# Performance work log

Hardware: AMD Instinct MI355X
Metric: run time of the kernel (lower is better)

## Reference

```python
import jax, jax.numpy as jnp
import numpy as np

NUM_HEADS = 16


def setup_inputs() -> dict:
    key = jax.random.key(0)
    ks = jax.random.split(key, 9)
    B, N, E = 2, 2048, 1024
    s = 1.0 / np.sqrt(E).astype(np.float32)
    inp = {"x": jax.random.normal(ks[0], (B, N, E), jnp.float32)}
    names = ["q", "k", "v", "o"]
    for i, n in enumerate(names):
        inp[f"W{n}"] = jax.random.normal(ks[1 + 2 * i], (E, E), jnp.float32) * s
        inp[f"b{n}"] = jax.random.normal(ks[2 + 2 * i], (E,), jnp.float32) * 0.01
    return inp


def _feature(x):
    # act_fun = '1+elu'
    return jax.nn.elu(x) + 1.0


def reference(x, Wq, bq, Wk, bk, Wv, bv, Wo, bo):
    B, N, E = x.shape
    H = NUM_HEADS
    d = E // H

    def proj(t, W, b):  # torch nn.Linear: t @ W^T + b
        return t @ W.T + b

    def split_heads(t):  # (B,N,E) -> (B,H,N,d)
        return t.reshape(B, N, H, d).transpose(0, 2, 1, 3)

    q = _feature(split_heads(proj(x, Wq, bq)))
    k = _feature(split_heads(proj(x, Wk, bk)))
    v = split_heads(proj(x, Wv, bv))

    # causal linear attention: o_t = q_t @ cumsum_{s<=t} (k_s v_s^T)
    kv = jnp.cumsum(k[..., :, None] * v[..., None, :], axis=2)  # (B,H,N,d,d)
    o = jnp.einsum('bhnd,bhnde->bhne', q, kv)                   # (B,H,N,d)

    o = o.transpose(0, 2, 1, 3).reshape(B, N, E)
    return o @ Wo.T + bo
```

## Files before the change

kernel.cpp:

```cpp
#include <hip/hip_runtime.h>
#include <hip/hip_bf16.h>
#include <cmath>

typedef unsigned short u16;
typedef __bf16 bf16x8 __attribute__((ext_vector_type(8)));
typedef float  f32x4  __attribute__((ext_vector_type(4)));
typedef float  f4     __attribute__((ext_vector_type(4)));
typedef u16    us4    __attribute__((ext_vector_type(4)));

#define DEVFN __device__ __forceinline__

static constexpr int Bq = 2, Nq = 2048, Eq = 1024;
static constexpr int Mq = Bq * Nq;
static constexpr int CHK = 64;
static constexpr int NC  = Nq / CHK;
static constexpr int BH  = Bq * 16;

DEVFN u16 f2b(float f) {
    union { float f; unsigned int u; } x; x.f = f;
    unsigned int r = x.u + 0x7fffu + ((x.u >> 16) & 1u);
    return (u16)(r >> 16);
}

DEVFN void gl_lds16(const u16* g, u16* l) {
    __builtin_amdgcn_global_load_lds(
        (const __attribute__((address_space(1))) unsigned int*)(g),
        (__attribute__((address_space(3))) unsigned int*)(l),
        16, 0, 0);
}

DEVFN const bf16x8* frag(const u16* S, int R, int G) {
    return reinterpret_cast<const bf16x8*>(&S[R * 64 + ((G ^ (R & 7)) << 3)]);
}

__global__ __launch_bounds__(256) void cvt_kernel(const float* __restrict__ src,
                                                  u16* __restrict__ dst, int n4) {
    int i = blockIdx.x * 256 + threadIdx.x;
    if (i < n4) {
        f4 v = *reinterpret_cast<const f4*>(&src[(size_t)i * 4]);
        us4 p; p[0] = f2b(v[0]); p[1] = f2b(v[1]); p[2] = f2b(v[2]); p[3] = f2b(v[3]);
        *reinterpret_cast<us4*>(&dst[(size_t)i * 4]) = p;
    }
}

__global__ __launch_bounds__(256) void cvt4_kernel(const float* __restrict__ s0,
                                                   const float* __restrict__ s1,
                                                   const float* __restrict__ s2,
                                                   const float* __restrict__ s3,
                                                   u16* __restrict__ dst, int n4each) {
    const int which = blockIdx.y;
    const float* s = (which == 0) ? s0 : (which == 1) ? s1 : (which == 2) ? s2 : s3;
    int i = blockIdx.x * 256 + threadIdx.x;
    if (i < n4each) {
        f4 v = *reinterpret_cast<const f4*>(&s[(size_t)i * 4]);
        us4 p; p[0] = f2b(v[0]); p[1] = f2b(v[1]); p[2] = f2b(v[2]); p[3] = f2b(v[3]);
        *reinterpret_cast<us4*>(&dst[((size_t)which * n4each + i) * 4]) = p;
    }
}

template<int MODE>
__global__ __launch_bounds__(256)
void gemm_kernel(const u16* __restrict__ X, const u16* __restrict__ W,
                 const float* __restrict__ b0, const float* __restrict__ b1,
                 const float* __restrict__ b2,
                 u16* __restrict__ Qb, u16* __restrict__ Kb, u16* __restrict__ KbT,
                 u16* __restrict__ VbT, float* __restrict__ outF)
{
    constexpr int BM = (MODE == 0) ? 128 : 64;
    constexpr int MI = BM / 32;
    __shared__ u16 As[BM * 64];
    __shared__ u16 Bs[128 * 64];
    const int tid  = threadIdx.x;
    const int m0   = blockIdx.y * BM, n0 = blockIdx.x * 128;
    const int wid  = tid >> 6, lane = tid & 63;
    const int wr   = (wid >> 1) * (BM / 2), wc = (wid & 1) * 64;
    const int fr   = lane & 15, fq = lane >> 4;

    const int srow = tid >> 3;
    const int sw   = (tid & 7) ^ (srow & 7);
    const u16* gA = X + (size_t)(m0 + srow) * 1024 + sw * 8;
    const u16* gB = W + (size_t)(n0 + srow) * 1024 + sw * 8;
    u16* lA = As + wid * 512;
    u16* lB = Bs + wid * 512;

    f32x4 acc[MI][4] = {};

    for (int k0 = 0; k0 < 1024; k0 += 64) {
        __syncthreads();
#pragma unroll
        for (int i = 0; i < BM / 32; ++i)
            gl_lds16(gA + k0 + i * 32 * 1024, lA + i * 2048);
#pragma unroll
        for (int i = 0; i < 4; ++i)
            gl_lds16(gB + k0 + i * 32 * 1024, lB + i * 2048);
        __syncthreads();

#pragma unroll
        for (int kk = 0; kk < 2; ++kk) {
            bf16x8 af[MI], bfv[4];
#pragma unroll
            for (int mi = 0; mi < MI; ++mi)
                af[mi] = *frag(As, wr + mi * 16 + fr, kk * 4 + fq);
#pragma unroll
            for (int ni = 0; ni < 4; ++ni)
                bfv[ni] = *frag(Bs, wc + ni * 16 + fr, kk * 4 + fq);
#pragma unroll
            for (int mi = 0; mi < MI; ++mi)
#pragma unroll
                for (int ni = 0; ni < 4; ++ni)
                    acc[mi][ni] = __builtin_amdgcn_mfma_f32_16x16x32_bf16(
                        af[mi], bfv[ni], acc[mi][ni], 0, 0, 0);
        }
    }

    if (MODE == 0) {
        const int seg = n0 >> 10;
        const float* bp = (seg == 0) ? b0 : (seg == 1) ? b1 : b2;
#pragma unroll
        for (int mi = 0; mi < MI; ++mi)
#pragma unroll
            for (int ni = 0; ni < 4; ++ni) {
                const int nl    = (n0 & 1023) + wc + ni * 16 + fr;
                const int mbase = m0 + wr + mi * 16 + fq * 4;
                const float bn  = bp[nl];
                float vr[4];
#pragma unroll
                for (int r = 0; r < 4; ++r) {
                    float v = acc[mi][ni][r] + bn;
                    if (seg < 2) v = (v > 0.f) ? (v + 1.f) : __expf(v);
                    vr[r] = v;
                }
                if (seg == 0) {
#pragma unroll
                    for (int r = 0; r < 4; ++r)
                        Qb[(size_t)(mbase + r) * 1024 + nl] = f2b(vr[r]);
                } else {
                    us4 pk;
#pragma unroll
                    for (int r = 0; r < 4; ++r) pk[r] = f2b(vr[r]);
                    const int bb = mbase >> 11, nt = mbase & 2047;
                    const int hh = nl >> 6,     dd = nl & 63;
                    u16* T = (seg == 1) ? KbT : VbT;
                    *reinterpret_cast<us4*>(
                        &T[((size_t)(bb * 16 + hh) * 64 + dd) * 2048 + nt]) = pk;
                    if (seg == 1) {
#pragma unroll
                        for (int r = 0; r < 4; ++r)
                            Kb[(size_t)(mbase + r) * 1024 + nl] = f2b(vr[r]);
                    }
                }
            }
    } else {
#pragma unroll
        for (int mi = 0; mi < MI; ++mi)
#pragma unroll
            for (int ni = 0; ni < 4; ++ni) {
                const int n     = n0 + wc + ni * 16 + fr;
                const int mbase = m0 + wr + mi * 16 + fq * 4;
                const float bn  = b0[n];
#pragma unroll
                for (int r = 0; r < 4; ++r)
                    outF[(size_t)(mbase + r) * 1024 + n] = acc[mi][ni][r] + bn;
            }
    }
}

__global__ __launch_bounds__(64)
void chunk_kv_kernel(const u16* __restrict__ KbT, const u16* __restrict__ VbT,
                     float* __restrict__ KVT)
{
    const int blk = blockIdx.x;
    const int bh = blk >> 5, c = blk & 31;
    const int lane = threadIdx.x;
    const int fr = lane & 15, fq = lane >> 4, fk = fq * 8;
    const u16* kt = KbT + (size_t)bh * 64 * 2048;
    const u16* vt = VbT + (size_t)bh * 64 * 2048;

    bf16x8 a[4][2], b[4][2];
#pragma unroll
    for (int mi = 0; mi < 4; ++mi)
#pragma unroll
        for (int kh = 0; kh < 2; ++kh)
            a[mi][kh] = *reinterpret_cast<const bf16x8*>(
                &vt[(size_t)(mi * 16 + fr) * 2048 + c * 64 + kh * 32 + fk]);
#pragma unroll
    for (int ni = 0; ni < 4; ++ni)
#pragma unroll
        for (int kh = 0; kh < 2; ++kh)
            b[ni][kh] = *reinterpret_cast<const bf16x8*>(
                &kt[(size_t)(ni * 16 + fr) * 2048 + c * 64 + kh * 32 + fk]);

    f32x4 acc[4][4] = {};
#pragma unroll
    for (int mi = 0; mi < 4; ++mi)
#pragma unroll
        for (int ni = 0; ni < 4; ++ni)
#pragma unroll
            for (int kh = 0; kh < 2; ++kh)
                acc[mi][ni] = __builtin_amdgcn_mfma_f32_16x16x32_bf16(
                    a[mi][kh], b[ni][kh], acc[mi][ni], 0, 0, 0);

    float* out = KVT + (size_t)blk * 4096;
#pragma unroll
    for (int mi = 0; mi < 4; ++mi)
#pragma unroll
        for (int ni = 0; ni < 4; ++ni)
#pragma unroll
            for (int r = 0; r < 4; ++r)
                out[(mi * 16 + fq * 4 + r) * 64 + ni * 16 + fr] = acc[mi][ni][r];
}

__global__ __launch_bounds__(256)
void scan_kernel(const float* __restrict__ KVT, u16* __restrict__ STb)
{
    const int bh = blockIdx.x >> 4, sl = blockIdx.x & 15;
    const int el = sl * 256 + threadIdx.x;
    const float* src = KVT + (size_t)bh * NC * 4096 + el;
    u16*         dst = STb + (size_t)bh * NC * 4096 + el;
    float run = 0.f;
#pragma unroll 4
    for (int c = 0; c < NC; ++c) {
        dst[(size_t)c * 4096] = f2b(run);
        run += src[(size_t)c * 4096];
    }
}

__global__ __launch_bounds__(64)
void attn_kernel(const u16* __restrict__ Qb, const u16* __restrict__ Kb,
                 const u16* __restrict__ VbT, const u16* __restrict__ STb,
                 u16* __restrict__ Ob)
{
    __shared__ u16 P[64 * 72];
    const int blk = blockIdx.x;
    const int bh = blk >> 5, c = blk & 31;
    const int b = bh >> 4, h = bh & 15;
    const int lane = threadIdx.x;
    const int fr = lane & 15, fq = lane >> 4, fk = fq * 8;
    const int tok0 = b * 2048 + c * 64;

    bf16x8 qa[4][2];
#pragma unroll
    for (int mi = 0; mi < 4; ++mi)
#pragma unroll
        for (int kh = 0; kh < 2; ++kh)
            qa[mi][kh] = *reinterpret_cast<const bf16x8*>(
                &Qb[(size_t)(tok0 + mi * 16 + fr) * 1024 + h * 64 + kh * 32 + fk]);

    {
        bf16x8 kb[4][2];
#pragma unroll
        for (int si = 0; si < 4; ++si)
#pragma unroll
            for (int kh = 0; kh < 2; ++kh)
                kb[si][kh] = *reinterpret_cast<const bf16x8*>(
                    &Kb[(size_t)(tok0 + si * 16 + fr) * 1024 + h * 64 + kh * 32 + fk]);
        f32x4 p[4][4] = {};
#pragma unroll
        for (int mi = 0; mi < 4; ++mi)
#pragma unroll
            for (int si = 0; si < 4; ++si)
#pragma unroll
                for (int kh = 0; kh < 2; ++kh)
                    p[mi][si] = __builtin_amdgcn_mfma_f32_16x16x32_bf16(
                        qa[mi][kh], kb[si][kh], p[mi][si], 0, 0, 0);
#pragma unroll
        for (int mi = 0; mi < 4; ++mi)
#pragma unroll
            for (int si = 0; si < 4; ++si)
#pragma unroll
                for (int r = 0; r < 4; ++r) {
                    int t = mi * 16 + fq * 4 + r;
                    int s = si * 16 + fr;
                    float v = (s <= t) ? p[mi][si][r] : 0.0f;
                    P[t * 72 + s] = f2b(v);
                }
    }
    __syncthreads();

    f32x4 acc[4][4] = {};
    {
        const u16* st = STb + (size_t)blk * 4096;
        bf16x8 sb[4][2];
#pragma unroll
        for (int ni = 0; ni < 4; ++ni)
#pragma unroll
            for (int kh = 0; kh < 2; ++kh)
                sb[ni][kh] = *reinterpret_cast<const bf16x8*>(
                    &st[(ni * 16 + fr) * 64 + kh * 32 + fk]);
#pragma unroll
        for (int mi = 0; mi < 4; ++mi)
#pragma unroll
            for (int ni = 0; ni < 4; ++ni)
#pragma unroll
                for (int kh = 0; kh < 2; ++kh)
                    acc[mi][ni] = __builtin_amdgcn_mfma_f32_16x16x32_bf16(
                        qa[mi][kh], sb[ni][kh], acc[mi][ni], 0, 0, 0);
    }
    {
        const u16* vt = VbT + (size_t)bh * 64 * 2048;
#pragma unroll
        for (int sh = 0; sh < 2; ++sh) {
            bf16x8 pa[4], vb[4];
#pragma unroll
            for (int mi = 0; mi < 4; ++mi)
                pa[mi] = *reinterpret_cast<const bf16x8*>(
                    &P[(mi * 16 + fr) * 72 + sh * 32 + fk]);
#pragma unroll
            for (int ni = 0; ni < 4; ++ni)
                vb[ni] = *reinterpret_cast<const bf16x8*>(
                    &vt[(size_t)(ni * 16 + fr) * 2048 + c * 64 + sh * 32 + fk]);
#pragma unroll
            for (int mi = 0; mi < 4; ++mi)
#pragma unroll
                for (int ni = 0; ni < 4; ++ni)
                    acc[mi][ni] = __builtin_amdgcn_mfma_f32_16x16x32_bf16(
                        pa[mi], vb[ni], acc[mi][ni], 0, 0, 0);
        }
    }
#pragma unroll
    for (int mi = 0; mi < 4; ++mi)
#pragma unroll
        for (int ni = 0; ni < 4; ++ni)
#pragma unroll
            for (int r = 0; r < 4; ++r) {
                int t = tok0 + mi * 16 + fq * 4 + r;
                int n = h * 64 + ni * 16 + fr;
                Ob[(size_t)t * 1024 + n] = f2b(acc[mi][ni][r]);
            }
}

extern "C" void kernel_launch(void* const* d_in, const int* in_sizes, int n_in,
                              void* d_out, int out_size, void* d_ws, size_t ws_size,
                              hipStream_t stream)
{
    (void)in_sizes; (void)n_in; (void)out_size; (void)ws_size;
    const float* x  = (const float*)d_in[0];
    const float* Wq = (const float*)d_in[1];
    const float* bq = (const float*)d_in[2];
    const float* Wk = (const float*)d_in[3];
    const float* bk = (const float*)d_in[4];
    const float* Wv = (const float*)d_in[5];
    const float* bv = (const float*)d_in[6];
    const float* Wo = (const float*)d_in[7];
    const float* bo = (const float*)d_in[8];
    float* out = (float*)d_out;

    char* ws = (char*)d_ws;
    constexpr size_t SZ_ME = (size_t)Mq * Eq * 2;
    u16*   Qb  = (u16*)  (ws + 0 * SZ_ME);
    u16*   Kb  = (u16*)  (ws + 1 * SZ_ME);
    u16*   KbT = (u16*)  (ws + 2 * SZ_ME);
    u16*   VbT = (u16*)  (ws + 3 * SZ_ME);
    u16*   Ob  = (u16*)  (ws + 4 * SZ_ME);
    float* KVT = (float*)(ws + 5 * SZ_ME);
    u16*   STb = (u16*)  (ws + 5 * SZ_ME + (size_t)BH * NC * 4096 * 4);
    u16*   Xb  = (u16*)  (ws + 6 * SZ_ME + (size_t)BH * NC * 4096 * 4);
    u16*   Wb0 = (u16*)  (ws + 7 * SZ_ME + (size_t)BH * NC * 4096 * 4);
    u16* Wqkvb = Wb0;
    u16* Wob   = Wb0 + (size_t)3 * Eq * Eq;

    {
        int n4x = Mq * Eq / 4;
        cvt_kernel<<<dim3((n4x + 255) / 256), dim3(256), 0, stream>>>(x, Xb, n4x);
        int n4w = Eq * Eq / 4;
        cvt4_kernel<<<dim3((n4w + 255) / 256, 4), dim3(256), 0, stream>>>(
            Wq, Wk, Wv, Wo, Wb0, n4w);
    }

    gemm_kernel<0><<<dim3(24, 32), dim3(256), 0, stream>>>(
        Xb, Wqkvb, bq, bk, bv, Qb, Kb, KbT, VbT, nullptr);

    chunk_kv_kernel<<<dim3(BH * NC), dim3(64), 0, stream>>>(KbT, VbT, KVT);
    scan_kernel<<<dim3(BH * 16), dim3(256), 0, stream>>>(KVT, STb);
    attn_kernel<<<dim3(BH * NC), dim3(64), 0, stream>>>(Qb, Kb, VbT, STb, Ob);

    gemm_kernel<1><<<dim3(8, 64), dim3(256), 0, stream>>>(
        Ob, Wob, bo, nullptr, nullptr, nullptr, nullptr, nullptr, nullptr, out);
}
```

Measured before the change: 102.9 us.

## Triple-buffer GEMM loads, merge conversion kernels, store chunk KV in bf16

Replaces the single-buffered GEMM with a 3-stage LDS ring using K-tiles of 32, explicit vmcnt waits and one barrier per step, so global-to-LDS loads overlap MFMA work. It also remaps block IDs so blocks sharing an operand are grouped (XCD-aware order). The two fp32-to-bf16 conversion kernels become a single launch. The per-chunk KV outer products are now stored in bf16 rather than fp32, halving the scan's traffic at some cost in accumulation precision.

```diff
diff --git a/kernel.cpp b/kernel.cpp
--- a/kernel.cpp
+++ b/kernel.cpp
@@ -21,6 +21,9 @@
     unsigned int r = x.u + 0x7fffu + ((x.u >> 16) & 1u);
     return (u16)(r >> 16);
 }
+DEVFN float b2f(u16 v) {
+    union { unsigned int u; float f; } x; x.u = ((unsigned int)v) << 16; return x.f;
+}
 
 DEVFN void gl_lds16(const u16* g, u16* l) {
     __builtin_amdgcn_global_load_lds(
@@ -29,89 +32,114 @@
         16, 0, 0);
 }
 
-DEVFN const bf16x8* frag(const u16* S, int R, int G) {
-    return reinterpret_cast<const bf16x8*>(&S[R * 64 + ((G ^ (R & 7)) << 3)]);
-}
-
-__global__ __launch_bounds__(256) void cvt_kernel(const float* __restrict__ src,
-                                                  u16* __restrict__ dst, int n4) {
-    int i = blockIdx.x * 256 + threadIdx.x;
-    if (i < n4) {
-        f4 v = *reinterpret_cast<const f4*>(&src[(size_t)i * 4]);
-        us4 p; p[0] = f2b(v[0]); p[1] = f2b(v[1]); p[2] = f2b(v[2]); p[3] = f2b(v[3]);
-        *reinterpret_cast<us4*>(&dst[(size_t)i * 4]) = p;
-    }
-}
-
-__global__ __launch_bounds__(256) void cvt4_kernel(const float* __restrict__ s0,
-                                                   const float* __restrict__ s1,
-                                                   const float* __restrict__ s2,
-                                                   const float* __restrict__ s3,
-                                                   u16* __restrict__ dst, int n4each) {
-    const int which = blockIdx.y;
-    const float* s = (which == 0) ? s0 : (which == 1) ? s1 : (which == 2) ? s2 : s3;
-    int i = blockIdx.x * 256 + threadIdx.x;
-    if (i < n4each) {
-        f4 v = *reinterpret_cast<const f4*>(&s[(size_t)i * 4]);
-        us4 p; p[0] = f2b(v[0]); p[1] = f2b(v[1]); p[2] = f2b(v[2]); p[3] = f2b(v[3]);
-        *reinterpret_cast<us4*>(&dst[((size_t)which * n4each + i) * 4]) = p;
-    }
+__global__ __launch_bounds__(256)
+void cvt_all_kernel(const float* __restrict__ x,
+                    const float* __restrict__ w0, const float* __restrict__ w1,
+                    const float* __restrict__ w2, const float* __restrict__ w3,
+                    u16* __restrict__ Xb, u16* __restrict__ Wb)
+{
+    const int blk = blockIdx.x;
+    const float* s; u16* d; int i;
+    if (blk < 4096) {
+        i = blk * 256 + threadIdx.x;  s = x;  d = Xb;
+    } else {
+        const int wsel = (blk - 4096) >> 10;
+        i = ((blk - 4096) & 1023) * 256 + threadIdx.x;
+        s = (wsel == 0) ? w0 : (wsel == 1) ? w1 : (wsel == 2) ? w2 : w3;
+        d = Wb + (size_t)wsel * (Eq * Eq);
+    }
+    f4 v = *reinterpret_cast<const f4*>(&s[(size_t)i * 4]);
+    us4 p; p[0] = f2b(v[0]); p[1] = f2b(v[1]); p[2] = f2b(v[2]); p[3] = f2b(v[3]);
+    *reinterpret_cast<us4*>(&d[(size_t)i * 4]) = p;
 }
 
 template<int MODE>
 __global__ __launch_bounds__(256)
-void gemm_kernel(const u16* __restrict__ X, const u16* __restrict__ W,
-                 const float* __restrict__ b0, const float* __restrict__ b1,
-                 const float* __restrict__ b2,
-                 u16* __restrict__ Qb, u16* __restrict__ Kb, u16* __restrict__ KbT,
-                 u16* __restrict__ VbT, float* __restrict__ outF)
-{
-    constexpr int BM = (MODE == 0) ? 128 : 64;
-    constexpr int MI = BM / 32;
-    __shared__ u16 As[BM * 64];
-    __shared__ u16 Bs[128 * 64];
-    const int tid  = threadIdx.x;
-    const int m0   = blockIdx.y * BM, n0 = blockIdx.x * 128;
-    const int wid  = tid >> 6, lane = tid & 63;
-    const int wr   = (wid >> 1) * (BM / 2), wc = (wid & 1) * 64;
-    const int fr   = lane & 15, fq = lane >> 4;
-
-    const int srow = tid >> 3;
-    const int sw   = (tid & 7) ^ (srow & 7);
-    const u16* gA = X + (size_t)(m0 + srow) * 1024 + sw * 8;
-    const u16* gB = W + (size_t)(n0 + srow) * 1024 + sw * 8;
-    u16* lA = As + wid * 512;
-    u16* lB = Bs + wid * 512;
+void gemm_ring(const u16* __restrict__ X, const u16* __restrict__ W,
+               const float* __restrict__ b0, const float* __restrict__ b1,
+               const float* __restrict__ b2,
+               u16* __restrict__ Qb, u16* __restrict__ Kb, u16* __restrict__ KbT,
+               u16* __restrict__ VbT, float* __restrict__ outF)
+{
+    constexpr int BM  = (MODE == 0) ? 128 : 64;
+    constexpr int MI  = BM / 32;
+    constexpr int AI  = BM / 64;
+    constexpr int BUF = BM * 32 + 4096;
+    constexpr int NT  = 32;
+    __shared__ u16 lds[3 * BUF];
+
+    const int tid = threadIdx.x, wid = tid >> 6, lane = tid & 63;
+    const int fid = (MODE == 0) ? ((blockIdx.x & 7) * 96 + (blockIdx.x >> 3))
+                                : ((blockIdx.x & 7) * 64 + (blockIdx.x >> 3));
+    const int bx  = (MODE == 0) ? (fid % 24) : (fid & 7);
+    const int by  = (MODE == 0) ? (fid / 24) : (fid >> 3);
+    const int m0  = by * BM, n0 = bx * 128;
+    const int wr  = (wid >> 1) * (BM / 2), wc = (wid & 1) * 64;
+    const int fr  = lane & 15, fq = lane >> 4;
+
+    const int srow0 = tid >> 2;
+    const int scol  = ((tid & 3) ^ (srow0 & 3)) * 8;
+    const u16* gA = X + (size_t)(m0 + srow0) * 1024 + scol;
+    const u16* gB = W + (size_t)(n0 + srow0) * 1024 + scol;
+    const int dA = wid * 512;
+    const int dB = BM * 32 + wid * 512;
+
+    const int fsw = (fq ^ (fr & 3)) << 3;
+    int aoff[MI], boff[4];
+#pragma unroll
+    for (int mi = 0; mi < MI; ++mi) aoff[mi] = (wr + mi * 16 + fr) * 32 + fsw;
+#pragma unroll
+    for (int ni = 0; ni < 4; ++ni)  boff[ni] = BM * 32 + (wc + ni * 16 + fr) * 32 + fsw;
+
+#define STAGE(kt, bsel) do {                                                   \
+        const int _k = (kt) * 32;                                              \
+        u16* _b = lds + (bsel) * BUF;                                          \
+        _Pragma("unroll")                                                      \
+        for (int it = 0; it < AI; ++it)                                        \
+            gl_lds16(gA + _k + (size_t)it * 64 * 1024, _b + dA + it * 2048);   \
+        _Pragma("unroll")                                                      \
+        for (int it = 0; it < 2; ++it)                                         \
+            gl_lds16(gB + _k + (size_t)it * 64 * 1024, _b + dB + it * 2048);   \
+    } while (0)
+
+    STAGE(0, 0);
+    STAGE(1, 1);
+    if (MODE == 0) asm volatile("s_waitcnt vmcnt(4)" ::: "memory");
+    else           asm volatile("s_waitcnt vmcnt(3)" ::: "memory");
+    __builtin_amdgcn_s_barrier();
+    __builtin_amdgcn_sched_barrier(0);
 
     f32x4 acc[MI][4] = {};
-
-    for (int k0 = 0; k0 < 1024; k0 += 64) {
-        __syncthreads();
-#pragma unroll
-        for (int i = 0; i < BM / 32; ++i)
-            gl_lds16(gA + k0 + i * 32 * 1024, lA + i * 2048);
-#pragma unroll
-        for (int i = 0; i < 4; ++i)
-            gl_lds16(gB + k0 + i * 32 * 1024, lB + i * 2048);
-        __syncthreads();
-
-#pragma unroll
-        for (int kk = 0; kk < 2; ++kk) {
-            bf16x8 af[MI], bfv[4];
-#pragma unroll
-            for (int mi = 0; mi < MI; ++mi)
-                af[mi] = *frag(As, wr + mi * 16 + fr, kk * 4 + fq);
+    int cb = 0, sb = 2;
+
+    for (int t = 0; t < NT; ++t) {
+        if (t + 2 < NT) STAGE(t + 2, sb);
+        const u16* buf = lds + cb * BUF;
+        bf16x8 af[MI], bfv[4];
+#pragma unroll
+        for (int mi = 0; mi < MI; ++mi)
+            af[mi] = *reinterpret_cast<const bf16x8*>(&buf[aoff[mi]]);
+#pragma unroll
+        for (int ni = 0; ni < 4; ++ni)
+            bfv[ni] = *reinterpret_cast<const bf16x8*>(&buf[boff[ni]]);
+#pragma unroll
+        for (int mi = 0; mi < MI; ++mi)
 #pragma unroll
             for (int ni = 0; ni < 4; ++ni)
-                bfv[ni] = *frag(Bs, wc + ni * 16 + fr, kk * 4 + fq);
-#pragma unroll
-            for (int mi = 0; mi < MI; ++mi)
-#pragma unroll
-                for (int ni = 0; ni < 4; ++ni)
-                    acc[mi][ni] = __builtin_amdgcn_mfma_f32_16x16x32_bf16(
-                        af[mi], bfv[ni], acc[mi][ni], 0, 0, 0);
+                acc[mi][ni] = __builtin_amdgcn_mfma_f32_16x16x32_bf16(
+                    af[mi], bfv[ni], acc[mi][ni], 0, 0, 0);
+        if (t < NT - 2) {
+            if (MODE == 0) asm volatile("s_waitcnt vmcnt(4)" ::: "memory");
+            else           asm volatile("s_waitcnt vmcnt(3)" ::: "memory");
+        } else if (t == NT - 2) {
+            asm volatile("s_waitcnt vmcnt(0)" ::: "memory");
         }
-    }
+        __builtin_amdgcn_s_barrier();
+        __builtin_amdgcn_sched_barrier(0);
+        cb = (cb == 2) ? 0 : cb + 1;
+        sb = (sb == 2) ? 0 : sb + 1;
+    }
+#undef STAGE
 
     if (MODE == 0) {
         const int seg = n0 >> 10;
@@ -167,7 +195,7 @@
 
 __global__ __launch_bounds__(64)
 void chunk_kv_kernel(const u16* __restrict__ KbT, const u16* __restrict__ VbT,
-                     float* __restrict__ KVT)
+                     u16* __restrict__ KVT)
 {
     const int blk = blockIdx.x;
     const int bh = blk >> 5, c = blk & 31;
@@ -200,28 +228,28 @@
                 acc[mi][ni] = __builtin_amdgcn_mfma_f32_16x16x32_bf16(
                     a[mi][kh], b[ni][kh], acc[mi][ni], 0, 0, 0);
 
-    float* out = KVT + (size_t)blk * 4096;
+    u16* out = KVT + (size_t)blk * 4096;
 #pragma unroll
     for (int mi = 0; mi < 4; ++mi)
 #pragma unroll
         for (int ni = 0; ni < 4; ++ni)
 #pragma unroll
             for (int r = 0; r < 4; ++r)
-                out[(mi * 16 + fq * 4 + r) * 64 + ni * 16 + fr] = acc[mi][ni][r];
+                out[(mi * 16 + fq * 4 + r) * 64 + ni * 16 + fr] = f2b(acc[mi][ni][r]);
 }
 
 __global__ __launch_bounds__(256)
-void scan_kernel(const float* __restrict__ KVT, u16* __restrict__ STb)
+void scan_kernel(const u16* __restrict__ KVT, u16* __restrict__ STb)
 {
     const int bh = blockIdx.x >> 4, sl = blockIdx.x & 15;
     const int el = sl * 256 + threadIdx.x;
-    const float* src = KVT + (size_t)bh * NC * 4096 + el;
-    u16*         dst = STb + (size_t)bh * NC * 4096 + el;
+    const u16* src = KVT + (size_t)bh * NC * 4096 + el;
+    u16*      dst  = STb + (size_t)bh * NC * 4096 + el;
     float run = 0.f;
 #pragma unroll 4
     for (int c = 0; c < NC; ++c) {
         dst[(size_t)c * 4096] = f2b(run);
-        run += src[(size_t)c * 4096];
+        run += b2f(src[(size_t)c * 4096]);
     }
 }
 
@@ -352,28 +380,22 @@
     u16*   KbT = (u16*)  (ws + 2 * SZ_ME);
     u16*   VbT = (u16*)  (ws + 3 * SZ_ME);
     u16*   Ob  = (u16*)  (ws + 4 * SZ_ME);
-    float* KVT = (float*)(ws + 5 * SZ_ME);
-    u16*   STb = (u16*)  (ws + 5 * SZ_ME + (size_t)BH * NC * 4096 * 4);
-    u16*   Xb  = (u16*)  (ws + 6 * SZ_ME + (size_t)BH * NC * 4096 * 4);
-    u16*   Wb0 = (u16*)  (ws + 7 * SZ_ME + (size_t)BH * NC * 4096 * 4);
+    u16*   KVT = (u16*)  (ws + 5 * SZ_ME);
+    u16*   STb = (u16*)  (ws + 6 * SZ_ME);
+    u16*   Xb  = (u16*)  (ws + 7 * SZ_ME);
+    u16*   Wb0 = (u16*)  (ws + 8 * SZ_ME);
     u16* Wqkvb = Wb0;
     u16* Wob   = Wb0 + (size_t)3 * Eq * Eq;
 
-    {
-        int n4x = Mq * Eq / 4;
-        cvt_kernel<<<dim3((n4x + 255) / 256), dim3(256), 0, stream>>>(x, Xb, n4x);
-        int n4w = Eq * Eq / 4;
-        cvt4_kernel<<<dim3((n4w + 255) / 256, 4), dim3(256), 0, stream>>>(
-            Wq, Wk, Wv, Wo, Wb0, n4w);
-    }
-
-    gemm_kernel<0><<<dim3(24, 32), dim3(256), 0, stream>>>(
+    cvt_all_kernel<<<dim3(8192), dim3(256), 0, stream>>>(x, Wq, Wk, Wv, Wo, Xb, Wb0);
+
+    gemm_ring<0><<<dim3(768), dim3(256), 0, stream>>>(
         Xb, Wqkvb, bq, bk, bv, Qb, Kb, KbT, VbT, nullptr);
 
     chunk_kv_kernel<<<dim3(BH * NC), dim3(64), 0, stream>>>(KbT, VbT, KVT);
     scan_kernel<<<dim3(BH * 16), dim3(256), 0, stream>>>(KVT, STb);
     attn_kernel<<<dim3(BH * NC), dim3(64), 0, stream>>>(Qb, Kb, VbT, STb, Ob);
 
-    gemm_kernel<1><<<dim3(8, 64), dim3(256), 0, stream>>>(
+    gemm_ring<1><<<dim3(512), dim3(256), 0, stream>>>(
         Ob, Wob, bo, nullptr, nullptr, nullptr, nullptr, nullptr, nullptr, out);
 }
```

After: 92.23 us. -10.4%, faster.
